# Kernel optimization log

Hardware: AMD Instinct MI355X
Metric: run time of the kernel (lower is better)

Reference implementation:

```python
import jax, jax.numpy as jnp
import numpy as np

N_EMBD = 1024
N_EXPERTS = 8
TOP_K = 2
D_FF = 4 * N_EMBD


def setup_inputs() -> dict:
    key = jax.random.key(0)
    ks = jax.random.split(key, 6)
    B, S = 4, 2048
    s = 1.0 / np.sqrt(N_EMBD)
    sf = 1.0 / np.sqrt(D_FF)
    x = jax.random.normal(ks[0], (B, S, N_EMBD), dtype=jnp.float32)
    router_w = jax.random.uniform(ks[1], (N_EMBD, N_EXPERTS), minval=-s, maxval=s, dtype=jnp.float32)
    wfc = jax.random.uniform(ks[2], (N_EXPERTS, N_EMBD, D_FF), minval=-s, maxval=s, dtype=jnp.float32)
    bfc = jax.random.uniform(ks[3], (N_EXPERTS, D_FF), minval=-s, maxval=s, dtype=jnp.float32)
    wproj = jax.random.uniform(ks[4], (N_EXPERTS, D_FF, N_EMBD), minval=-sf, maxval=sf, dtype=jnp.float32)
    bproj = jax.random.uniform(ks[5], (N_EXPERTS, N_EMBD), minval=-sf, maxval=sf, dtype=jnp.float32)
    return {"x": x, "router_w": router_w, "wfc": wfc, "bfc": bfc, "wproj": wproj, "bproj": bproj}


def reference(x, router_w, wfc, bfc, wproj, bproj):
    B, S, D = x.shape
    E = wfc.shape[0]
    xf = x.reshape(-1, D)  # [N, D] tokens
    logits = xf @ router_w  # [N, E]
    probs = jax.nn.softmax(logits.astype(jnp.float32), axis=-1)
    w, sel = jax.lax.top_k(probs, TOP_K)  # [N, K]
    w = w / jnp.sum(w, axis=-1, keepdims=True)  # norm_topk_prob
    w = w.astype(x.dtype)
    out = jnp.zeros_like(xf)
    for e in range(E):
        # per-token gate for expert e (0 if not routed here) -- same math as
        # gather -> MLP -> weighted scatter-add in the original
        gate = jnp.sum(jnp.where(sel == e, w, jnp.zeros_like(w)), axis=-1)  # [N]
        h = jax.nn.gelu(xf @ wfc[e] + bfc[e], approximate=False)  # [N, 4D]
        y = h @ wproj[e] + bproj[e]  # [N, D]
        out = out + gate[:, None] * y
    return out.reshape(B, S, D)
```

## Files before the change

### kernel.cpp

```cpp
#include <hip/hip_runtime.h>
#include <hip/hip_bf16.h>


#define N_TOK 8192
#define DMODEL 1024
#define NEXP 8
#define DFF 4096
#define CAP 8192
#define MAXW 136

typedef __attribute__((ext_vector_type(8))) short short8;
typedef __attribute__((ext_vector_type(4))) float f32x4;

#define GLOAD_LDS16(g, l)                                              \
  __builtin_amdgcn_global_load_lds(                                    \
      (const __attribute__((address_space(1))) unsigned int*)(g),      \
      (__attribute__((address_space(3))) unsigned int*)(l), 16, 0, 0)

__device__ __forceinline__ unsigned short f2bf(float f) {
  unsigned u = __float_as_uint(f);
  return (unsigned short)((u + 0x7FFFu + ((u >> 16) & 1u)) >> 16);
}

__device__ __forceinline__ float gelu_f(float v) {
  return 0.5f * v * (1.0f + erff(v * 0.70710678118654752f));
}

__global__ void router_k(const float* __restrict__ x, const float* __restrict__ rw,
                         int* __restrict__ cnt, int* __restrict__ tok,
                         float* __restrict__ gate, unsigned short* __restrict__ xb) {
  int lane = threadIdx.x & 63;
  int t = blockIdx.x * 4 + (threadIdx.x >> 6);
  const float* xr = x + (size_t)t * DMODEL;
  unsigned short* xbr = xb + (size_t)t * DMODEL;
  float p[8];
#pragma unroll
  for (int e = 0; e < 8; ++e) p[e] = 0.0f;
#pragma unroll
  for (int j = 0; j < DMODEL / 64; ++j) {
    int i = lane + j * 64;
    float xv = xr[i];
    xbr[i] = f2bf(xv);
    const float4* r = (const float4*)(rw + (size_t)i * 8);
    float4 a = r[0], b = r[1];
    p[0] += xv * a.x; p[1] += xv * a.y; p[2] += xv * a.z; p[3] += xv * a.w;
    p[4] += xv * b.x; p[5] += xv * b.y; p[6] += xv * b.z; p[7] += xv * b.w;
  }
#pragma unroll
  for (int e = 0; e < 8; ++e) {
#pragma unroll
    for (int off = 32; off; off >>= 1) p[e] += __shfl_xor(p[e], off, 64);
  }
  if (lane == 0) {
    int e1 = 0;
#pragma unroll
    for (int e = 1; e < 8; ++e) if (p[e] > p[e1]) e1 = e;
    int e2 = (e1 == 0) ? 1 : 0;
#pragma unroll
    for (int e = 0; e < 8; ++e) if (e != e1 && p[e] > p[e2]) e2 = e;
    float w1 = 1.0f / (1.0f + expf(p[e2] - p[e1]));
    float w2 = 1.0f - w1;
    int s1 = atomicAdd(&cnt[e1], 1);
    tok[e1 * CAP + s1] = t; gate[e1 * CAP + s1] = w1;
    int s2 = atomicAdd(&cnt[e2], 1);
    tok[e2 * CAP + s2] = t; gate[e2 * CAP + s2] = w2;
  }
}

__global__ void prefix_k(const int* __restrict__ cnt, int* __restrict__ off,
                         int* __restrict__ nwork, int* __restrict__ wl) {
  if (threadIdx.x == 0 && blockIdx.x == 0) {
    int s = 0, n = 0;
    for (int e = 0; e < NEXP; ++e) {
      off[e] = s;
      int ntile = (cnt[e] + 127) >> 7;
      for (int mt = 0; mt < ntile; ++mt) wl[n++] = (e << 16) | mt;
      s += cnt[e];
    }
    nwork[0] = n;
  }
}

__global__ __launch_bounds__(256) void cvt_wt_k(const float* __restrict__ W,
                                                unsigned short* __restrict__ WT,
                                                int K, int N) {
  __shared__ float ls[64][68];
  int b = blockIdx.x;
  int nkt = K >> 6, nnt = N >> 6;
  int kt = b % nkt;
  int nt = (b / nkt) % nnt;
  int e = b / (nkt * nnt);
  const float* Wb = W + (size_t)e * K * N + (size_t)(kt * 64) * N + nt * 64;
  int t = threadIdx.x;
  int nn = (t & 15) * 4, kr = t >> 4;
#pragma unroll
  for (int i = 0; i < 4; ++i) {
    float4 v = *(const float4*)(Wb + (size_t)(kr + 16 * i) * N + nn);
    *(float4*)&ls[kr + 16 * i][nn] = v;
  }
  __syncthreads();
  int on = t >> 2, kc = (t & 3) * 16;
  unsigned short* dst = WT + (size_t)e * N * K + (size_t)(nt * 64 + on) * K + kt * 64 + kc;
  short8 r0, r1;
#pragma unroll
  for (int j = 0; j < 8; ++j) r0[j] = (short)f2bf(ls[kc + j][on]);
#pragma unroll
  for (int j = 0; j < 8; ++j) r1[j] = (short)f2bf(ls[kc + 8 + j][on]);
  *(short8*)dst = r0;
  *(short8*)(dst + 8) = r1;
}

#define STAGE(buf, kk)                                          \
  do {                                                          \
    GLOAD_LDS16(gA + (kk), &As[buf][(tid >> 2) * 32 + lc]);     \
    GLOAD_LDS16(gB + (kk), &Bs[buf][(tid >> 2) * 32 + lc]);     \
  } while (0)

#define COMPUTE(buf)                                                            \
  do {                                                                          \
    short8 af[4], bfv[2];                                                       \
    _Pragma("unroll") for (int i = 0; i < 4; ++i)                               \
        af[i] = *(const short8*)&As[buf][(wr * 64 + i * 16 + fr) * 32 + g * 8]; \
    _Pragma("unroll") for (int i = 0; i < 2; ++i)                               \
        bfv[i] = *(const short8*)&Bs[buf][(wc * 32 + i * 16 + fr) * 32 + g * 8];\
    _Pragma("unroll") for (int mi = 0; mi < 4; ++mi)                            \
        _Pragma("unroll") for (int ni = 0; ni < 2; ++ni)                        \
            acc[mi][ni] = __builtin_amdgcn_mfma_f32_16x16x32_bf16(              \
                af[mi], bfv[ni], acc[mi][ni], 0, 0, 0);                         \
  } while (0)

#define WAITV(n) asm volatile("s_waitcnt vmcnt(" #n ")" ::: "memory")
#define BAR() __builtin_amdgcn_s_barrier()

#define KLOOP(KTOT)                                                 \
  STAGE(0, 0);                                                      \
  STAGE(1, 32);                                                     \
  STAGE(2, 64);                                                     \
  {                                                                 \
    int cur = 0;                                                    \
    _Pragma("unroll 1") for (int k0 = 0; k0 + 96 < (KTOT); k0 += 32) {\
      WAITV(4);                                                     \
      BAR();                                                        \
      COMPUTE(cur);                                                 \
      BAR();                                                        \
      STAGE(cur, k0 + 96);                                          \
      cur = (cur == 2) ? 0 : cur + 1;                               \
    }                                                               \
    WAITV(4);                                                       \
    BAR();                                                          \
    COMPUTE(cur);                                                   \
    cur = (cur == 2) ? 0 : cur + 1;                                 \
    WAITV(2);                                                       \
    BAR();                                                          \
    COMPUTE(cur);                                                   \
    cur = (cur == 2) ? 0 : cur + 1;                                 \
    WAITV(0);                                                       \
    BAR();                                                          \
    COMPUTE(cur);                                                   \
  }

#define NT1 32
__global__ __launch_bounds__(512, 4) void gemm1a_k(
    const unsigned short* __restrict__ xb, const unsigned short* __restrict__ wT,
    const float* __restrict__ bfc, const int* __restrict__ cnt,
    const int* __restrict__ off, const int* __restrict__ tok,
    const int* __restrict__ nwork, const int* __restrict__ wl,
    unsigned short* __restrict__ h) {
  int bid = (int)(blockIdx.x & 7) * ((int)gridDim.x >> 3) + (int)(blockIdx.x >> 3);
  int widx = bid / NT1;
  int nt = bid % NT1;
  if (widx >= nwork[0]) return;
  int wle = wl[widx];
  int e = wle >> 16;
  int mt = wle & 0xffff;
  int Me = cnt[e];
  int base = off[e];
  int n0 = nt * 128;

  __shared__ __align__(16) unsigned short As[3][128 * 32];
  __shared__ __align__(16) unsigned short Bs[3][128 * 32];

  int tid = threadIdx.x;
  int lane = tid & 63, w = tid >> 6;
  int lc = (tid & 3) * 8;

  int ari = mt * 128 + (tid >> 2);
  int t0 = tok[e * CAP + ((ari < Me) ? ari : (Me - 1))];
  const unsigned short* gA = xb + (size_t)t0 * DMODEL + lc;
  const unsigned short* gB = wT + ((size_t)e * DFF + n0 + (tid >> 2)) * DMODEL + lc;

  int wr = w >> 2, wc = w & 3;
  int g = lane >> 4, fr = lane & 15;

  f32x4 acc[4][2];
#pragma unroll
  for (int i = 0; i < 4; ++i)
#pragma unroll
    for (int j = 0; j < 2; ++j) acc[i][j] = (f32x4)0.0f;

  KLOOP(DMODEL);

#pragma unroll
  for (int mi = 0; mi < 4; ++mi) {
    int rl = wr * 64 + mi * 16 + g * 4;
#pragma unroll
    for (int i = 0; i < 4; ++i) {
      int r = mt * 128 + rl + i;
      if (r < Me) {
        unsigned short* hrow = h + (size_t)(base + r) * DFF;
#pragma unroll
        for (int ni = 0; ni < 2; ++ni) {
          int col = n0 + wc * 32 + ni * 16 + fr;
          float v = acc[mi][ni][i] + bfc[e * DFF + col];
          hrow[col] = f2bf(gelu_f(v));
        }
      }
    }
  }
}

#define NT2 8
__global__ __launch_bounds__(512, 4) void gemm2a_k(
    const unsigned short* __restrict__ h, const unsigned short* __restrict__ wT,
    const float* __restrict__ bproj, const int* __restrict__ cnt,
    const int* __restrict__ off, const int* __restrict__ tok,
    const int* __restrict__ nwork, const int* __restrict__ wl,
    const float* __restrict__ gate, float* __restrict__ out) {
  int bid = (int)(blockIdx.x & 7) * ((int)gridDim.x >> 3) + (int)(blockIdx.x >> 3);
  int widx = bid / NT2;
  int nt = bid % NT2;
  if (widx >= nwork[0]) return;
  int wle = wl[widx];
  int e = wle >> 16;
  int mt = wle & 0xffff;
  int Me = cnt[e];
  int base = off[e];
  int n0 = nt * 128;

  __shared__ __align__(16) unsigned short As[3][128 * 32];
  __shared__ __align__(16) unsigned short Bs[3][128 * 32];

  int tid = threadIdx.x;
  int lane = tid & 63, w = tid >> 6;
  int lc = (tid & 3) * 8;

  const unsigned short* gA = h + (size_t)(base + mt * 128 + (tid >> 2)) * DFF + lc;
  const unsigned short* gB = wT + ((size_t)e * DMODEL + n0 + (tid >> 2)) * DFF + lc;

  int wr = w >> 2, wc = w & 3;
  int g = lane >> 4, fr = lane & 15;

  f32x4 acc[4][2];
#pragma unroll
  for (int i = 0; i < 4; ++i)
#pragma unroll
    for (int j = 0; j < 2; ++j) acc[i][j] = (f32x4)0.0f;

  KLOOP(DFF);

#pragma unroll
  for (int mi = 0; mi < 4; ++mi) {
    int rl = wr * 64 + mi * 16 + g * 4;
#pragma unroll
    for (int i = 0; i < 4; ++i) {
      int r = mt * 128 + rl + i;
      if (r < Me) {
        int tkn = tok[e * CAP + r];
        float gv = gate[e * CAP + r];
        float* orow = out + (size_t)tkn * DMODEL;
#pragma unroll
        for (int ni = 0; ni < 2; ++ni) {
          int col = n0 + wc * 32 + ni * 16 + fr;
          float v = acc[mi][ni][i] + bproj[e * DMODEL + col];
          atomicAdd(orow + col, gv * v);
        }
      }
    }
  }
}

extern "C" void kernel_launch(void* const* d_in, const int* in_sizes, int n_in,
                              void* d_out, int out_size, void* d_ws, size_t ws_size,
                              hipStream_t stream) {
  const float* x = (const float*)d_in[0];
  const float* rw = (const float*)d_in[1];
  const float* wfc = (const float*)d_in[2];
  const float* bfc = (const float*)d_in[3];
  const float* wproj = (const float*)d_in[4];
  const float* bproj = (const float*)d_in[5];
  float* out = (float*)d_out;

  char* ws = (char*)d_ws;
  int* cnt = (int*)ws;
  int* off_ = (int*)(ws + 64);
  int* nwork = (int*)(ws + 128);
  int* wl = (int*)(ws + 256);
  int* tok = (int*)(ws + 4096);
  float* gate = (float*)(ws + 4096 + (size_t)NEXP * CAP * 4);
  size_t HOFF = 4096 + 2 * (size_t)NEXP * CAP * 4;
  unsigned short* h = (unsigned short*)(ws + HOFF);
  size_t HSZ = (size_t)(16384 + 128) * DFF * 2;
  size_t XOFF = HOFF + HSZ;
  size_t WOFF = XOFF + (size_t)N_TOK * DMODEL * 2;
  size_t WSZ = (size_t)NEXP * DFF * DMODEL * 2;
  unsigned short* xb = (unsigned short*)(ws + XOFF);
  unsigned short* wT1 = (unsigned short*)(ws + WOFF);

  hipMemsetAsync(cnt, 0, 128, stream);
  hipMemsetAsync(out, 0, (size_t)out_size * 4, stream);
  router_k<<<N_TOK / 4, 256, 0, stream>>>(x, rw, cnt, tok, gate, xb);
  prefix_k<<<1, 64, 0, stream>>>(cnt, off_, nwork, wl);

  if (ws_size >= WOFF + 2 * WSZ) {
    unsigned short* wT2 = (unsigned short*)(ws + WOFF + WSZ);
    cvt_wt_k<<<NEXP * (DMODEL / 64) * (DFF / 64), 256, 0, stream>>>(wfc, wT1, DMODEL, DFF);
    cvt_wt_k<<<NEXP * (DFF / 64) * (DMODEL / 64), 256, 0, stream>>>(wproj, wT2, DFF, DMODEL);
    gemm1a_k<<<MAXW * NT1, 512, 0, stream>>>(xb, wT1, bfc, cnt, off_, tok, nwork, wl, h);
    gemm2a_k<<<MAXW * NT2, 512, 0, stream>>>(h, wT2, bproj, cnt, off_, tok, nwork, wl, gate, out);
  } else {
    cvt_wt_k<<<NEXP * (DMODEL / 64) * (DFF / 64), 256, 0, stream>>>(wfc, wT1, DMODEL, DFF);
    gemm1a_k<<<MAXW * NT1, 512, 0, stream>>>(xb, wT1, bfc, cnt, off_, tok, nwork, wl, h);
    cvt_wt_k<<<NEXP * (DFF / 64) * (DMODEL / 64), 256, 0, stream>>>(wproj, wT1, DFF, DMODEL);
    gemm2a_k<<<MAXW * NT2, 512, 0, stream>>>(h, wT1, bproj, cnt, off_, tok, nwork, wl, gate, out);
  }
}
```

Baseline: 768.9 us.

## Widen MoE GEMM tiles to 128x256 with swizzled LDS and unrolled pipeline

Both expert GEMM kernels now compute 128x256 output tiles instead of 128x128, doubling the B tile in LDS and the per-wave accumulators (4x4 MFMA fragments). The goal is more MFMA work per A-tile load and fewer blocks. An XOR swizzle on the LDS column offset is meant to cut bank conflicts on fragment reads. The K loop is unrolled by three with fixed buffer indices, and block ordering changes so N-tile is the slow index across work items. In exchange, register and LDS pressure rise (about 72KB LDS per block), which may lower occupancy under the 512x4 launch bounds, and the grid has fewer blocks to spread across CUs.

```diff
diff --git a/kernel.cpp b/kernel.cpp
--- a/kernel.cpp
+++ b/kernel.cpp
@@ -110,21 +110,22 @@
   *(short8*)(dst + 8) = r1;
 }
 
-#define STAGE(buf, kk)                                          \
-  do {                                                          \
-    GLOAD_LDS16(gA + (kk), &As[buf][(tid >> 2) * 32 + lc]);     \
-    GLOAD_LDS16(gB + (kk), &Bs[buf][(tid >> 2) * 32 + lc]);     \
+#define STAGE(buf, kk)                                                  \
+  do {                                                                  \
+    GLOAD_LDS16(gA + (kk), &As[buf][tid * 8]);                          \
+    GLOAD_LDS16(gB + (kk), &Bs[buf][tid * 8]);                          \
+    GLOAD_LDS16(gB2 + (kk), &Bs[buf][4096 + tid * 8]);                  \
   } while (0)
 
 #define COMPUTE(buf)                                                            \
   do {                                                                          \
-    short8 af[4], bfv[2];                                                       \
+    short8 af[4], bfv[4];                                                       \
     _Pragma("unroll") for (int i = 0; i < 4; ++i)                               \
-        af[i] = *(const short8*)&As[buf][(wr * 64 + i * 16 + fr) * 32 + g * 8]; \
-    _Pragma("unroll") for (int i = 0; i < 2; ++i)                               \
-        bfv[i] = *(const short8*)&Bs[buf][(wc * 32 + i * 16 + fr) * 32 + g * 8];\
+        af[i] = *(const short8*)&As[buf][(wr * 64 + i * 16 + fr) * 32 + co];    \
+    _Pragma("unroll") for (int i = 0; i < 4; ++i)                               \
+        bfv[i] = *(const short8*)&Bs[buf][(wc * 64 + i * 16 + fr) * 32 + co];   \
     _Pragma("unroll") for (int mi = 0; mi < 4; ++mi)                            \
-        _Pragma("unroll") for (int ni = 0; ni < 2; ++ni)                        \
+        _Pragma("unroll") for (int ni = 0; ni < 4; ++ni)                        \
             acc[mi][ni] = __builtin_amdgcn_mfma_f32_16x16x32_bf16(              \
                 af[mi], bfv[ni], acc[mi][ni], 0, 0, 0);                         \
   } while (0)
@@ -132,34 +133,26 @@
 #define WAITV(n) asm volatile("s_waitcnt vmcnt(" #n ")" ::: "memory")
 #define BAR() __builtin_amdgcn_s_barrier()
 
-#define KLOOP(KTOT)                                                 \
-  STAGE(0, 0);                                                      \
-  STAGE(1, 32);                                                     \
-  STAGE(2, 64);                                                     \
-  {                                                                 \
-    int cur = 0;                                                    \
-    _Pragma("unroll 1") for (int k0 = 0; k0 + 96 < (KTOT); k0 += 32) {\
-      WAITV(4);                                                     \
-      BAR();                                                        \
-      COMPUTE(cur);                                                 \
-      BAR();                                                        \
-      STAGE(cur, k0 + 96);                                          \
-      cur = (cur == 2) ? 0 : cur + 1;                               \
-    }                                                               \
-    WAITV(4);                                                       \
-    BAR();                                                          \
-    COMPUTE(cur);                                                   \
-    cur = (cur == 2) ? 0 : cur + 1;                                 \
-    WAITV(2);                                                       \
-    BAR();                                                          \
-    COMPUTE(cur);                                                   \
-    cur = (cur == 2) ? 0 : cur + 1;                                 \
-    WAITV(0);                                                       \
-    BAR();                                                          \
-    COMPUTE(cur);                                                   \
-  }
-
-#define NT1 32
+#define KLOOP(KTOT)                                                       \
+  STAGE(0, 0);                                                            \
+  STAGE(1, 32);                                                           \
+  STAGE(2, 64);                                                           \
+  {                                                                       \
+    int k0 = 0;                                                           \
+    _Pragma("unroll 1") for (int it = 0; it < ((KTOT) / 32 - 5) / 3; ++it) { \
+      WAITV(6); BAR(); COMPUTE(0); BAR(); STAGE(0, k0 + 96);              \
+      WAITV(6); BAR(); COMPUTE(1); BAR(); STAGE(1, k0 + 128);             \
+      WAITV(6); BAR(); COMPUTE(2); BAR(); STAGE(2, k0 + 160);             \
+      k0 += 96;                                                           \
+    }                                                                     \
+    WAITV(6); BAR(); COMPUTE(0); BAR(); STAGE(0, k0 + 96);                \
+    WAITV(6); BAR(); COMPUTE(1); BAR(); STAGE(1, k0 + 128);               \
+    WAITV(6); BAR(); COMPUTE(2);                                          \
+    WAITV(3); BAR(); COMPUTE(0);                                          \
+    WAITV(0); BAR(); COMPUTE(1);                                          \
+  }
+
+#define NT1 16
 __global__ __launch_bounds__(512, 4) void gemm1a_k(
     const unsigned short* __restrict__ xb, const unsigned short* __restrict__ wT,
     const float* __restrict__ bfc, const int* __restrict__ cnt,
@@ -167,36 +160,38 @@
     const int* __restrict__ nwork, const int* __restrict__ wl,
     unsigned short* __restrict__ h) {
   int bid = (int)(blockIdx.x & 7) * ((int)gridDim.x >> 3) + (int)(blockIdx.x >> 3);
-  int widx = bid / NT1;
-  int nt = bid % NT1;
+  int widx = bid % MAXW;
+  int nt = bid / MAXW;
   if (widx >= nwork[0]) return;
   int wle = wl[widx];
   int e = wle >> 16;
   int mt = wle & 0xffff;
   int Me = cnt[e];
   int base = off[e];
-  int n0 = nt * 128;
+  int n0 = nt * 256;
 
   __shared__ __align__(16) unsigned short As[3][128 * 32];
-  __shared__ __align__(16) unsigned short Bs[3][128 * 32];
+  __shared__ __align__(16) unsigned short Bs[3][256 * 32];
 
   int tid = threadIdx.x;
   int lane = tid & 63, w = tid >> 6;
-  int lc = (tid & 3) * 8;
+  int lc = (((tid & 3) ^ ((tid >> 2) & 3)) * 8);
 
   int ari = mt * 128 + (tid >> 2);
   int t0 = tok[e * CAP + ((ari < Me) ? ari : (Me - 1))];
   const unsigned short* gA = xb + (size_t)t0 * DMODEL + lc;
   const unsigned short* gB = wT + ((size_t)e * DFF + n0 + (tid >> 2)) * DMODEL + lc;
+  const unsigned short* gB2 = gB + (size_t)128 * DMODEL;
 
   int wr = w >> 2, wc = w & 3;
   int g = lane >> 4, fr = lane & 15;
-
-  f32x4 acc[4][2];
+  int co = ((g ^ (fr & 3)) * 8);
+
+  f32x4 acc[4][4];
 #pragma unroll
   for (int i = 0; i < 4; ++i)
 #pragma unroll
-    for (int j = 0; j < 2; ++j) acc[i][j] = (f32x4)0.0f;
+    for (int j = 0; j < 4; ++j) acc[i][j] = (f32x4)0.0f;
 
   KLOOP(DMODEL);
 
@@ -209,8 +204,8 @@
       if (r < Me) {
         unsigned short* hrow = h + (size_t)(base + r) * DFF;
 #pragma unroll
-        for (int ni = 0; ni < 2; ++ni) {
-          int col = n0 + wc * 32 + ni * 16 + fr;
+        for (int ni = 0; ni < 4; ++ni) {
+          int col = n0 + wc * 64 + ni * 16 + fr;
           float v = acc[mi][ni][i] + bfc[e * DFF + col];
           hrow[col] = f2bf(gelu_f(v));
         }
@@ -219,7 +214,7 @@
   }
 }
 
-#define NT2 8
+#define NT2 4
 __global__ __launch_bounds__(512, 4) void gemm2a_k(
     const unsigned short* __restrict__ h, const unsigned short* __restrict__ wT,
     const float* __restrict__ bproj, const int* __restrict__ cnt,
@@ -227,34 +222,36 @@
     const int* __restrict__ nwork, const int* __restrict__ wl,
     const float* __restrict__ gate, float* __restrict__ out) {
   int bid = (int)(blockIdx.x & 7) * ((int)gridDim.x >> 3) + (int)(blockIdx.x >> 3);
-  int widx = bid / NT2;
-  int nt = bid % NT2;
+  int widx = bid % MAXW;
+  int nt = bid / MAXW;
   if (widx >= nwork[0]) return;
   int wle = wl[widx];
   int e = wle >> 16;
   int mt = wle & 0xffff;
   int Me = cnt[e];
   int base = off[e];
-  int n0 = nt * 128;
+  int n0 = nt * 256;
 
   __shared__ __align__(16) unsigned short As[3][128 * 32];
-  __shared__ __align__(16) unsigned short Bs[3][128 * 32];
+  __shared__ __align__(16) unsigned short Bs[3][256 * 32];
 
   int tid = threadIdx.x;
   int lane = tid & 63, w = tid >> 6;
-  int lc = (tid & 3) * 8;
+  int lc = (((tid & 3) ^ ((tid >> 2) & 3)) * 8);
 
   const unsigned short* gA = h + (size_t)(base + mt * 128 + (tid >> 2)) * DFF + lc;
   const unsigned short* gB = wT + ((size_t)e * DMODEL + n0 + (tid >> 2)) * DFF + lc;
+  const unsigned short* gB2 = gB + (size_t)128 * DFF;
 
   int wr = w >> 2, wc = w & 3;
   int g = lane >> 4, fr = lane & 15;
-
-  f32x4 acc[4][2];
+  int co = ((g ^ (fr & 3)) * 8);
+
+  f32x4 acc[4][4];
 #pragma unroll
   for (int i = 0; i < 4; ++i)
 #pragma unroll
-    for (int j = 0; j < 2; ++j) acc[i][j] = (f32x4)0.0f;
+    for (int j = 0; j < 4; ++j) acc[i][j] = (f32x4)0.0f;
 
   KLOOP(DFF);
 
@@ -269,8 +266,8 @@
         float gv = gate[e * CAP + r];
         float* orow = out + (size_t)tkn * DMODEL;
 #pragma unroll
-        for (int ni = 0; ni < 2; ++ni) {
-          int col = n0 + wc * 32 + ni * 16 + fr;
+        for (int ni = 0; ni < 4; ++ni) {
+          int col = n0 + wc * 64 + ni * 16 + fr;
           float v = acc[mi][ni][i] + bproj[e * DMODEL + col];
           atomicAdd(orow + col, gv * v);
         }
```

Result: slower. 815.0 us (+6.0%).
